# Performance work log

Measured on AMD Instinct MI355X. Metric: run time of the kernel, lower is better.

Reference implementation:

```python
import jax, jax.numpy as jnp
import numpy as np

INPUT_SIZE = 1024
HIDDEN_SIZE = 1024

def _xavier(key, shape):
    fan_in, fan_out = shape
    limit = np.sqrt(6.0 / (fan_in + fan_out))
    return jax.random.uniform(key, shape, jnp.float32, -limit, limit)

def setup_inputs() -> dict:
    key = jax.random.key(0)
    ks = jax.random.split(key, 9)
    x = jax.random.normal(ks[0], (64, 512, INPUT_SIZE), jnp.float32)
    d = {"x": x}
    names_i = ["W_ii", "W_fi", "W_gi", "W_oi"]
    names_h = ["W_ih", "W_fh", "W_gh", "W_oh"]
    for n, k in zip(names_i, ks[1:5]):
        d[n] = _xavier(k, (INPUT_SIZE, HIDDEN_SIZE))
    for n, k in zip(names_h, ks[5:9]):
        d[n] = _xavier(k, (HIDDEN_SIZE, HIDDEN_SIZE))
    for n in ["b_ii", "b_ih", "b_fi", "b_fh", "b_gi", "b_gh", "b_oi", "b_oh"]:
        d[n] = jnp.zeros((HIDDEN_SIZE,), jnp.float32)
    return d

def _lstm(x, W_ii, W_ih, b_ii, b_ih, W_fi, W_fh, b_fi, b_fh,
          W_gi, W_gh, b_gi, b_gh, W_oi, W_oh, b_oi, b_oh):
    B, S, _ = x.shape
    H = W_ih.shape[0]
    # Fuse the 4 input-side GEMMs into one and hoist out of the recurrence.
    Wi = jnp.concatenate([W_ii, W_fi, W_gi, W_oi], axis=1)          # [I, 4H]
    Wh = jnp.concatenate([W_ih, W_fh, W_gh, W_oh], axis=1)          # [H, 4H]
    bi = jnp.concatenate([b_ii + b_ih, b_fi + b_fh, b_gi + b_gh, b_oi + b_oh])
    xproj = jnp.einsum('bsi,ig->bsg', x, Wi) + bi                    # [B, S, 4H]

    def step(carry, xp_t):
        h, c = carry
        gates = xp_t + h @ Wh                                        # [B, 4H]
        i_t = jax.nn.sigmoid(gates[:, 0 * H:1 * H])
        f_t = jax.nn.sigmoid(gates[:, 1 * H:2 * H])
        g_t = jnp.tanh(gates[:, 2 * H:3 * H])
        o_t = jax.nn.sigmoid(gates[:, 3 * H:4 * H])
        c = f_t * c + i_t * g_t
        h = o_t * jnp.tanh(c)
        return (h, c), None

    h0 = jnp.zeros((B, H), x.dtype)
    c0 = jnp.zeros((B, H), x.dtype)
    (h_t, c_t), _ = jax.lax.scan(step, (h0, c0), jnp.swapaxes(xproj, 0, 1))
    return h_t, c_t

def reference(x, W_ii, W_ih, b_ii, b_ih, W_fi, W_fh, b_fi, b_fh,
              W_gi, W_gh, b_gi, b_gh, W_oi, W_oh, b_oi, b_oh):
    return _lstm(x, W_ii, W_ih, b_ii, b_ih, W_fi, W_fh, b_fi, b_fh,
                 W_gi, W_gh, b_gi, b_gh, W_oi, W_oh, b_oi, b_oh)
```

## Files before the change

kernel.cpp:

```cpp
#include <hip/hip_runtime.h>
#include <hip/hip_bf16.h>

#define SEQ   512
#define HID   1024
#define NBLK  256
#define NTHR  256
#define PADK  2056
#define GPS   36

typedef __attribute__((ext_vector_type(8))) short bf16x8;
typedef __attribute__((ext_vector_type(4))) float f32x4;
typedef __attribute__((ext_vector_type(2))) float f32x2;

struct Params {
  const float* x;
  const float* Wi[4];
  const float* Wh[4];
  const float* bi[4];
  const float* bh[4];
  float* out;
  const short* xbf;
  short* hb0;
  short* hb1;
  unsigned* arrive;
  unsigned* gen;
};

__device__ __forceinline__ float sig_(float v)  { return 1.0f / (1.0f + __expf(-v)); }
__device__ __forceinline__ float tanh_(float v) { return 1.0f - 2.0f / (__expf(2.0f * v) + 1.0f); }

__device__ __forceinline__ short f2b(float f) {
  unsigned u = __builtin_bit_cast(unsigned, f);
  u += 0x7FFFu + ((u >> 16) & 1u);
  return (short)(u >> 16);
}
__device__ __forceinline__ bf16x8 cvt8(const float* p) {
  f32x4 a = *(const f32x4*)p;
  f32x4 b = *(const f32x4*)(p + 4);
  bf16x8 r;
  r[0] = f2b(a[0]); r[1] = f2b(a[1]); r[2] = f2b(a[2]); r[3] = f2b(a[3]);
  r[4] = f2b(b[0]); r[5] = f2b(b[1]); r[6] = f2b(b[2]); r[7] = f2b(b[3]);
  return r;
}

__device__ __forceinline__ bf16x8 ld16_sc1(const short* p) {
  bf16x8 r;
  asm volatile("global_load_dwordx4 %0, %1, off sc1" : "=v"(r) : "v"(p));
  return r;
}
__device__ __forceinline__ void wait_vm0() {
  asm volatile("s_waitcnt vmcnt(0)" ::: "memory");
}

__global__ __launch_bounds__(256) void init_ws(unsigned* bar, unsigned* hzero, int hn) {
  int i = blockIdx.x * blockDim.x + threadIdx.x;
  if (i < 8448) bar[i] = 0u;
  if (i < hn) hzero[i] = 0u;
}

__global__ __launch_bounds__(256) void cvt_x(const float* __restrict__ x,
                                             short* __restrict__ xb) {
  size_t i = ((size_t)blockIdx.x * 256 + threadIdx.x) * 8;
  *(bf16x8*)(xb + i) = cvt8(x + i);
}

__device__ __forceinline__ void gbar_fence(unsigned* arrive, unsigned* gen,
                                           int tid, int bid, unsigned tgt) {
  __syncthreads();
  if (bid == 0) {
    if (tid != 0) {
      int polls = 0;
      while (__hip_atomic_load(&arrive[tid * 32], __ATOMIC_RELAXED,
                               __HIP_MEMORY_SCOPE_AGENT) < tgt) {
        __builtin_amdgcn_s_sleep(1);
        if (++polls > (1 << 22)) break;
      }
    }
    __syncthreads();
    if (tid == 0) {
      __threadfence();
      __hip_atomic_store(gen, tgt, __ATOMIC_RELEASE, __HIP_MEMORY_SCOPE_AGENT);
    }
    __syncthreads();
  } else {
    if (tid == 0) {
      __threadfence();
      __hip_atomic_store(&arrive[bid * 32], tgt, __ATOMIC_RELEASE,
                         __HIP_MEMORY_SCOPE_AGENT);
      int polls = 0;
      while (__hip_atomic_load(gen, __ATOMIC_RELAXED,
                               __HIP_MEMORY_SCOPE_AGENT) < tgt) {
        __builtin_amdgcn_s_sleep(1);
        if (++polls > (1 << 22)) break;
      }
      __threadfence();
    }
    __syncthreads();
  }
}

template <bool FULL>
__global__ __launch_bounds__(NTHR, 1) void lstm_persistent(Params p) {
  extern __shared__ char smem[];
  short* bls    = (short*)smem;
  float* gparts = (float*)(smem + 131584);
  float* cst    = (float*)(smem + 131584 + 18432);
  float* bias_s = (float*)(smem + 131584 + 18432 + 1024);

  const int tid = threadIdx.x;
  const int bid = blockIdx.x;
  const int cg  = bid & 127;
  const int mh  = bid >> 7;
  const int r0  = mh * 32;
  const int j0  = cg * 8;

  {
    const int g    = tid & 3;
    const int krow = tid >> 2;
    const float* wi = p.Wi[g];
    const float* wh = p.Wh[g];
    for (int kb = 0; kb < 2048; kb += 64) {
      int k = kb + krow;
      const float* src = (k < HID) ? (wi + (size_t)k * HID + j0)
                                   : (wh + (size_t)(k - HID) * HID + j0);
      f32x4 va = *(const f32x4*)src;
      f32x4 vb = *(const f32x4*)(src + 4);
      #pragma unroll
      for (int jj = 0; jj < 4; ++jj) {
        bls[(4 * jj + g) * PADK + k]       = f2b(va[jj]);
        bls[(4 * (jj + 4) + g) * PADK + k] = f2b(vb[jj]);
      }
    }
  }
  if (tid < 32) {
    int g = tid & 3, j = j0 + (tid >> 2);
    bias_s[tid] = p.bi[g][j] + p.bh[g][j];
  }
  if (tid < 128) { cst[2 * tid] = 0.0f; cst[2 * tid + 1] = 0.0f; }
  __syncthreads();

  const int lane = tid & 63;
  const int ksl  = tid >> 6;
  const int m16  = lane & 15;
  const int quad = lane >> 4;
  const size_t rm0 = (size_t)(r0 + m16);
  const size_t rm1 = (size_t)(r0 + 16 + m16);
  const short* bB0 = bls + (size_t)m16 * PADK + ksl * 512 + quad * 8;
  const short* bB1 = bls + (size_t)(16 + m16) * PADK + ksl * 512 + quad * 8;

  const unsigned* myflag =
      p.arrive + (size_t)(mh * 128 + (ksl - 2) * 64 + lane) * 32;

  float cfin0 = 0.0f, cfin1 = 0.0f;

  for (int t = 0; t < SEQ; ++t) {
    f32x4 acc00 = {0,0,0,0}, acc01 = {0,0,0,0};
    f32x4 acc10 = {0,0,0,0}, acc11 = {0,0,0,0};

    if constexpr (FULL) {
      if (ksl < 2) {
        const short* xb = p.xbf + ksl * 512 + quad * 8 + (size_t)t * HID;
        const short* pa0 = xb + rm0 * (SEQ * HID);
        const short* pa1 = xb + rm1 * (SEQ * HID);
        #pragma unroll 4
        for (int ki = 0; ki < 16; ++ki) {
          bf16x8 a0 = *(const bf16x8*)(pa0 + ki * 32);
          bf16x8 a1 = *(const bf16x8*)(pa1 + ki * 32);
          bf16x8 b0 = *(const bf16x8*)(bB0 + ki * 32);
          bf16x8 b1 = *(const bf16x8*)(bB1 + ki * 32);
          acc00 = __builtin_amdgcn_mfma_f32_16x16x32_bf16(a0, b0, acc00, 0, 0, 0);
          acc01 = __builtin_amdgcn_mfma_f32_16x16x32_bf16(a0, b1, acc01, 0, 0, 0);
          acc10 = __builtin_amdgcn_mfma_f32_16x16x32_bf16(a1, b0, acc10, 0, 0, 0);
          acc11 = __builtin_amdgcn_mfma_f32_16x16x32_bf16(a1, b1, acc11, 0, 0, 0);
        }
      } else {
        if (t > 0) {
          int polls = 0;
          while (__hip_atomic_load(myflag, __ATOMIC_RELAXED,
                                   __HIP_MEMORY_SCOPE_AGENT) < (unsigned)t) {
            __builtin_amdgcn_s_sleep(1);
            if (++polls > (1 << 22)) break;
          }
        }
        const short* hr = ((t & 1) ? p.hb1 : p.hb0) + (ksl - 2) * 512 + quad * 8;
        const short* pa0 = hr + rm0 * HID;
        const short* pa1 = hr + rm1 * HID;
        bf16x8 A0[16], A1[16];
        #pragma unroll
        for (int ki = 0; ki < 16; ++ki) {
          A0[ki] = ld16_sc1(pa0 + ki * 32);
          A1[ki] = ld16_sc1(pa1 + ki * 32);
        }
        wait_vm0();
        #pragma unroll
        for (int ki = 0; ki < 16; ++ki) {
          asm volatile("" : "+v"(A0[ki]));
          asm volatile("" : "+v"(A1[ki]));
        }
        #pragma unroll
        for (int ki = 0; ki < 16; ++ki) {
          bf16x8 b0 = *(const bf16x8*)(bB0 + ki * 32);
          bf16x8 b1 = *(const bf16x8*)(bB1 + ki * 32);
          acc00 = __builtin_amdgcn_mfma_f32_16x16x32_bf16(A0[ki], b0, acc00, 0, 0, 0);
          acc01 = __builtin_amdgcn_mfma_f32_16x16x32_bf16(A0[ki], b1, acc01, 0, 0, 0);
          acc10 = __builtin_amdgcn_mfma_f32_16x16x32_bf16(A1[ki], b0, acc10, 0, 0, 0);
          acc11 = __builtin_amdgcn_mfma_f32_16x16x32_bf16(A1[ki], b1, acc11, 0, 0, 0);
        }
      }
    } else {
      const float *fa0, *fa1;
      if (ksl < 2) {
        const float* xb = p.x + ksl * 512 + quad * 8 + (size_t)t * HID;
        fa0 = xb + rm0 * (SEQ * HID);
        fa1 = xb + rm1 * (SEQ * HID);
      } else {
        const float* hr = (p.out + ((t & 1) ? 65536 : 0)) + (ksl - 2) * 512 + quad * 8;
        fa0 = hr + rm0 * HID;
        fa1 = hr + rm1 * HID;
      }
      #pragma unroll 2
      for (int ki = 0; ki < 16; ++ki) {
        bf16x8 a0 = cvt8(fa0 + ki * 32);
        bf16x8 a1 = cvt8(fa1 + ki * 32);
        bf16x8 b0 = *(const bf16x8*)(bB0 + ki * 32);
        bf16x8 b1 = *(const bf16x8*)(bB1 + ki * 32);
        acc00 = __builtin_amdgcn_mfma_f32_16x16x32_bf16(a0, b0, acc00, 0, 0, 0);
        acc01 = __builtin_amdgcn_mfma_f32_16x16x32_bf16(a0, b1, acc01, 0, 0, 0);
        acc10 = __builtin_amdgcn_mfma_f32_16x16x32_bf16(a1, b0, acc10, 0, 0, 0);
        acc11 = __builtin_amdgcn_mfma_f32_16x16x32_bf16(a1, b1, acc11, 0, 0, 0);
      }
    }

    {
      float* gp = gparts + ksl * (32 * GPS);
      #pragma unroll
      for (int r = 0; r < 4; ++r) {
        gp[(quad * 4 + r) * GPS + m16]           = acc00[r];
        gp[(quad * 4 + r) * GPS + 16 + m16]      = acc01[r];
        gp[(16 + quad * 4 + r) * GPS + m16]      = acc10[r];
        gp[(16 + quad * 4 + r) * GPS + 16 + m16] = acc11[r];
      }
    }
    __syncthreads();

    if (tid < 128) {
      int rl = tid >> 2, jp = tid & 3;
      f32x4 ga = {0,0,0,0}, gb = {0,0,0,0};
      #pragma unroll
      for (int s = 0; s < 4; ++s) {
        const float* gp = gparts + s * (32 * GPS) + rl * GPS + jp * 8;
        ga += *(const f32x4*)gp;
        gb += *(const f32x4*)(gp + 4);
      }
      f32x4 ba = *(const f32x4*)(bias_s + jp * 8);
      f32x4 bb = *(const f32x4*)(bias_s + jp * 8 + 4);

      float i0 = sig_(ga[0] + ba[0]);
      float f0 = sig_(ga[1] + ba[1]);
      float g0 = tanh_(ga[2] + ba[2]);
      float o0 = sig_(ga[3] + ba[3]);
      float i1 = sig_(gb[0] + bb[0]);
      float f1 = sig_(gb[1] + bb[1]);
      float g1 = tanh_(gb[2] + bb[2]);
      float o1 = sig_(gb[3] + bb[3]);

      int ci = rl * 8 + jp * 2;
      float c0 = f0 * cst[ci]     + i0 * g0;
      float c1 = f1 * cst[ci + 1] + i1 * g1;
      cst[ci] = c0; cst[ci + 1] = c1;
      float h0v = o0 * tanh_(c0);
      float h1v = o1 * tanh_(c1);

      size_t off = (size_t)(r0 + rl) * HID + j0 + jp * 2;
      if constexpr (FULL) {
        short* hw = (t & 1) ? p.hb0 : p.hb1;
        unsigned u = (unsigned)(unsigned short)f2b(h0v) |
                     ((unsigned)(unsigned short)f2b(h1v) << 16);
        __hip_atomic_store((unsigned*)(hw + off), u, __ATOMIC_RELAXED,
                           __HIP_MEMORY_SCOPE_AGENT);
        if (t == SEQ - 1) {
          f32x2 hv = {h0v, h1v}; *(f32x2*)(p.out + off) = hv;
          f32x2 cv = {c0, c1};   *(f32x2*)(p.out + 65536 + off) = cv;
        }
      } else {
        float* hw = p.out + ((t & 1) ? 0 : 65536);
        f32x2 hv = {h0v, h1v};
        *(f32x2*)(hw + off) = hv;
        if (t == SEQ - 1) { cfin0 = c0; cfin1 = c1; }
      }
    }

    if constexpr (FULL) {
      __syncthreads();
      if (t < SEQ - 1 && tid == 0)
        __hip_atomic_store(&p.arrive[bid * 32], (unsigned)(t + 1),
                           __ATOMIC_RELAXED, __HIP_MEMORY_SCOPE_AGENT);
    } else {
      if (t < SEQ - 1)
        gbar_fence(p.arrive, p.gen, tid, bid, (unsigned)(t + 1));
    }
  }

  if constexpr (!FULL) {
    if (tid < 128) {
      int rl = tid >> 2, jp = tid & 3;
      size_t off = (size_t)(r0 + rl) * HID + j0 + jp * 2;
      f32x2 cv = {cfin0, cfin1};
      *(f32x2*)(p.out + 65536 + off) = cv;
    }
  }
}

extern "C" void kernel_launch(void* const* d_in, const int* in_sizes, int n_in,
                              void* d_out, int out_size, void* d_ws, size_t ws_size,
                              hipStream_t stream) {
  Params prm;
  prm.x = (const float*)d_in[0];
  for (int g = 0; g < 4; ++g) {
    prm.Wi[g] = (const float*)d_in[1 + g];
    prm.Wh[g] = (const float*)d_in[5 + g];
    prm.bi[g] = (const float*)d_in[9 + 2 * g];
    prm.bh[g] = (const float*)d_in[10 + 2 * g];
  }
  prm.out    = (float*)d_out;
  prm.arrive = (unsigned*)d_ws;
  prm.gen    = prm.arrive + 8192;
  prm.xbf = nullptr; prm.hb0 = nullptr; prm.hb1 = nullptr;

  const size_t need_full = 65536 + 67108864 + 2 * 131072;
  const bool full = ws_size >= need_full;
  if (full) {
    prm.xbf = (const short*)((char*)d_ws + 65536);
    prm.hb0 = (short*)((char*)d_ws + 65536 + 67108864);
    prm.hb1 = prm.hb0 + 65536;
  }

  const int smem_bytes = 131584 + 18432 + 1024 + 128;
  hipFuncSetAttribute((const void*)lstm_persistent<true>,
                      hipFuncAttributeMaxDynamicSharedMemorySize, smem_bytes);
  hipFuncSetAttribute((const void*)lstm_persistent<false>,
                      hipFuncAttributeMaxDynamicSharedMemorySize, smem_bytes);

  if (full) {
    init_ws<<<256, 256, 0, stream>>>((unsigned*)d_ws, (unsigned*)prm.hb0, 32768);
    cvt_x<<<16384, 256, 0, stream>>>(prm.x, (short*)prm.xbf);
    lstm_persistent<true><<<NBLK, NTHR, smem_bytes, stream>>>(prm);
  } else {
    init_ws<<<256, 256, 0, stream>>>((unsigned*)d_ws, (unsigned*)d_out, 65536);
    lstm_persistent<false><<<NBLK, NTHR, smem_bytes, stream>>>(prm);
  }
}
```

Baseline: 3.687 ms.

## Replace double-buffered h with per-step ring and drop x bf16 pre-conversion

Removes the separate cvt_x pass: x is read as fp32 and converted to bf16 inside the recurrence loop. It also replaces the ping-pong h buffers with a ring holding one slot per timestep. Because no slot is ever overwritten, h loads can drop the sc1 cache-bypass modifier and go through the normal cache path. The cost is twice as many bytes of x read per step, plus inline conversion work and a larger workspace requirement (512 slots).

```diff
diff --git a/kernel.cpp b/kernel.cpp
--- a/kernel.cpp
+++ b/kernel.cpp
@@ -7,6 +7,7 @@
 #define NTHR  256
 #define PADK  2056
 #define GPS   36
+#define RSLOT 65792
 
 typedef __attribute__((ext_vector_type(8))) short bf16x8;
 typedef __attribute__((ext_vector_type(4))) float f32x4;
@@ -19,9 +20,7 @@
   const float* bi[4];
   const float* bh[4];
   float* out;
-  const short* xbf;
-  short* hb0;
-  short* hb1;
+  short* hring;
   unsigned* arrive;
   unsigned* gen;
 };
@@ -43,9 +42,9 @@
   return r;
 }
 
-__device__ __forceinline__ bf16x8 ld16_sc1(const short* p) {
+__device__ __forceinline__ bf16x8 ld16_l2(const short* p) {
   bf16x8 r;
-  asm volatile("global_load_dwordx4 %0, %1, off sc1" : "=v"(r) : "v"(p));
+  asm volatile("global_load_dwordx4 %0, %1, off" : "=v"(r) : "v"(p));
   return r;
 }
 __device__ __forceinline__ void wait_vm0() {
@@ -56,12 +55,6 @@
   int i = blockIdx.x * blockDim.x + threadIdx.x;
   if (i < 8448) bar[i] = 0u;
   if (i < hn) hzero[i] = 0u;
-}
-
-__global__ __launch_bounds__(256) void cvt_x(const float* __restrict__ x,
-                                             short* __restrict__ xb) {
-  size_t i = ((size_t)blockIdx.x * 256 + threadIdx.x) * 8;
-  *(bf16x8*)(xb + i) = cvt8(x + i);
 }
 
 __device__ __forceinline__ void gbar_fence(unsigned* arrive, unsigned* gen,
@@ -159,13 +152,13 @@
 
     if constexpr (FULL) {
       if (ksl < 2) {
-        const short* xb = p.xbf + ksl * 512 + quad * 8 + (size_t)t * HID;
-        const short* pa0 = xb + rm0 * (SEQ * HID);
-        const short* pa1 = xb + rm1 * (SEQ * HID);
+        const float* xb = p.x + ksl * 512 + quad * 8 + (size_t)t * HID;
+        const float* fa0 = xb + rm0 * (SEQ * HID);
+        const float* fa1 = xb + rm1 * (SEQ * HID);
         #pragma unroll 4
         for (int ki = 0; ki < 16; ++ki) {
-          bf16x8 a0 = *(const bf16x8*)(pa0 + ki * 32);
-          bf16x8 a1 = *(const bf16x8*)(pa1 + ki * 32);
+          bf16x8 a0 = cvt8(fa0 + ki * 32);
+          bf16x8 a1 = cvt8(fa1 + ki * 32);
           bf16x8 b0 = *(const bf16x8*)(bB0 + ki * 32);
           bf16x8 b1 = *(const bf16x8*)(bB1 + ki * 32);
           acc00 = __builtin_amdgcn_mfma_f32_16x16x32_bf16(a0, b0, acc00, 0, 0, 0);
@@ -182,14 +175,15 @@
             if (++polls > (1 << 22)) break;
           }
         }
-        const short* hr = ((t & 1) ? p.hb1 : p.hb0) + (ksl - 2) * 512 + quad * 8;
+        const short* hr = p.hring + (size_t)t * RSLOT
+                        + (ksl - 2) * 512 + quad * 8;
         const short* pa0 = hr + rm0 * HID;
         const short* pa1 = hr + rm1 * HID;
         bf16x8 A0[16], A1[16];
         #pragma unroll
         for (int ki = 0; ki < 16; ++ki) {
-          A0[ki] = ld16_sc1(pa0 + ki * 32);
-          A1[ki] = ld16_sc1(pa1 + ki * 32);
+          A0[ki] = ld16_l2(pa0 + ki * 32);
+          A1[ki] = ld16_l2(pa1 + ki * 32);
         }
         wait_vm0();
         #pragma unroll
@@ -273,12 +267,13 @@
 
       size_t off = (size_t)(r0 + rl) * HID + j0 + jp * 2;
       if constexpr (FULL) {
-        short* hw = (t & 1) ? p.hb0 : p.hb1;
-        unsigned u = (unsigned)(unsigned short)f2b(h0v) |
-                     ((unsigned)(unsigned short)f2b(h1v) << 16);
-        __hip_atomic_store((unsigned*)(hw + off), u, __ATOMIC_RELAXED,
-                           __HIP_MEMORY_SCOPE_AGENT);
-        if (t == SEQ - 1) {
+        if (t < SEQ - 1) {
+          short* hw = p.hring + (size_t)(t + 1) * RSLOT;
+          unsigned u = (unsigned)(unsigned short)f2b(h0v) |
+                       ((unsigned)(unsigned short)f2b(h1v) << 16);
+          __hip_atomic_store((unsigned*)(hw + off), u, __ATOMIC_RELAXED,
+                             __HIP_MEMORY_SCOPE_AGENT);
+        } else {
           f32x2 hv = {h0v, h1v}; *(f32x2*)(p.out + off) = hv;
           f32x2 cv = {c0, c1};   *(f32x2*)(p.out + 65536 + off) = cv;
         }
@@ -325,15 +320,11 @@
   prm.out    = (float*)d_out;
   prm.arrive = (unsigned*)d_ws;
   prm.gen    = prm.arrive + 8192;
-  prm.xbf = nullptr; prm.hb0 = nullptr; prm.hb1 = nullptr;
-
-  const size_t need_full = 65536 + 67108864 + 2 * 131072;
+  prm.hring  = nullptr;
+
+  const size_t need_full = 65536 + (size_t)SEQ * (size_t)RSLOT * 2;
   const bool full = ws_size >= need_full;
-  if (full) {
-    prm.xbf = (const short*)((char*)d_ws + 65536);
-    prm.hb0 = (short*)((char*)d_ws + 65536 + 67108864);
-    prm.hb1 = prm.hb0 + 65536;
-  }
+  if (full) prm.hring = (short*)((char*)d_ws + 65536);
 
   const int smem_bytes = 131584 + 18432 + 1024 + 128;
   hipFuncSetAttribute((const void*)lstm_persistent<true>,
@@ -342,8 +333,7 @@
                       hipFuncAttributeMaxDynamicSharedMemorySize, smem_bytes);
 
   if (full) {
-    init_ws<<<256, 256, 0, stream>>>((unsigned*)d_ws, (unsigned*)prm.hb0, 32768);
-    cvt_x<<<16384, 256, 0, stream>>>(prm.x, (short*)prm.xbf);
+    init_ws<<<256, 256, 0, stream>>>((unsigned*)d_ws, (unsigned*)prm.hring, 32768);
     lstm_persistent<true><<<NBLK, NTHR, smem_bytes, stream>>>(prm);
   } else {
     init_ws<<<256, 256, 0, stream>>>((unsigned*)d_ws, (unsigned*)d_out, 65536);
```

Result: slower. 4.541 ms (+23.2%).

## Use per-timestep hidden-state ring buffer with plain loads and packed arrive flags

Applied to the files above, without the earlier changes.

Adds a mode that writes each step's bf16 hidden state into a separate ring slot, so readers can use ordinary cached global loads instead of sc1 loads. Fresh addresses each step avoid stale-cache hazards without bypass bits. It also packs the per-block arrive flags contiguously instead of spacing them 128 bytes apart. The cost is a larger workspace (512 slots), and the flag packing changes cache-line sharing among pollers and writers.

```diff
diff --git a/kernel.cpp b/kernel.cpp
--- a/kernel.cpp
+++ b/kernel.cpp
@@ -7,6 +7,7 @@
 #define NTHR  256
 #define PADK  2056
 #define GPS   36
+#define RSLOT 65792
 
 typedef __attribute__((ext_vector_type(8))) short bf16x8;
 typedef __attribute__((ext_vector_type(4))) float f32x4;
@@ -20,6 +21,7 @@
   const float* bh[4];
   float* out;
   const short* xbf;
+  short* hring;
   short* hb0;
   short* hb1;
   unsigned* arrive;
@@ -46,6 +48,11 @@
 __device__ __forceinline__ bf16x8 ld16_sc1(const short* p) {
   bf16x8 r;
   asm volatile("global_load_dwordx4 %0, %1, off sc1" : "=v"(r) : "v"(p));
+  return r;
+}
+__device__ __forceinline__ bf16x8 ld16_l2(const short* p) {
+  bf16x8 r;
+  asm volatile("global_load_dwordx4 %0, %1, off" : "=v"(r) : "v"(p));
   return r;
 }
 __device__ __forceinline__ void wait_vm0() {
@@ -99,7 +106,7 @@
   }
 }
 
-template <bool FULL>
+template <int MODE>
 __global__ __launch_bounds__(NTHR, 1) void lstm_persistent(Params p) {
   extern __shared__ char smem[];
   short* bls    = (short*)smem;
@@ -149,7 +156,7 @@
   const short* bB1 = bls + (size_t)(16 + m16) * PADK + ksl * 512 + quad * 8;
 
   const unsigned* myflag =
-      p.arrive + (size_t)(mh * 128 + (ksl - 2) * 64 + lane) * 32;
+      p.arrive + (size_t)(mh * 128 + (ksl - 2) * 64 + lane);
 
   float cfin0 = 0.0f, cfin1 = 0.0f;
 
@@ -157,7 +164,7 @@
     f32x4 acc00 = {0,0,0,0}, acc01 = {0,0,0,0};
     f32x4 acc10 = {0,0,0,0}, acc11 = {0,0,0,0};
 
-    if constexpr (FULL) {
+    if constexpr (MODE >= 1) {
       if (ksl < 2) {
         const short* xb = p.xbf + ksl * 512 + quad * 8 + (size_t)t * HID;
         const short* pa0 = xb + rm0 * (SEQ * HID);
@@ -182,14 +189,23 @@
             if (++polls > (1 << 22)) break;
           }
         }
-        const short* hr = ((t & 1) ? p.hb1 : p.hb0) + (ksl - 2) * 512 + quad * 8;
+        const short* hr;
+        if constexpr (MODE == 2)
+          hr = p.hring + (size_t)t * RSLOT + (ksl - 2) * 512 + quad * 8;
+        else
+          hr = ((t & 1) ? p.hb1 : p.hb0) + (ksl - 2) * 512 + quad * 8;
         const short* pa0 = hr + rm0 * HID;
         const short* pa1 = hr + rm1 * HID;
         bf16x8 A0[16], A1[16];
         #pragma unroll
         for (int ki = 0; ki < 16; ++ki) {
-          A0[ki] = ld16_sc1(pa0 + ki * 32);
-          A1[ki] = ld16_sc1(pa1 + ki * 32);
+          if constexpr (MODE == 2) {
+            A0[ki] = ld16_l2(pa0 + ki * 32);
+            A1[ki] = ld16_l2(pa1 + ki * 32);
+          } else {
+            A0[ki] = ld16_sc1(pa0 + ki * 32);
+            A1[ki] = ld16_sc1(pa1 + ki * 32);
+          }
         }
         wait_vm0();
         #pragma unroll
@@ -272,13 +288,18 @@
       float h1v = o1 * tanh_(c1);
 
       size_t off = (size_t)(r0 + rl) * HID + j0 + jp * 2;
-      if constexpr (FULL) {
-        short* hw = (t & 1) ? p.hb0 : p.hb1;
+      if constexpr (MODE >= 1) {
         unsigned u = (unsigned)(unsigned short)f2b(h0v) |
                      ((unsigned)(unsigned short)f2b(h1v) << 16);
-        __hip_atomic_store((unsigned*)(hw + off), u, __ATOMIC_RELAXED,
-                           __HIP_MEMORY_SCOPE_AGENT);
-        if (t == SEQ - 1) {
+        if (t < SEQ - 1) {
+          short* hw;
+          if constexpr (MODE == 2)
+            hw = p.hring + (size_t)(t + 1) * RSLOT;
+          else
+            hw = (t & 1) ? p.hb0 : p.hb1;
+          __hip_atomic_store((unsigned*)(hw + off), u, __ATOMIC_RELAXED,
+                             __HIP_MEMORY_SCOPE_AGENT);
+        } else {
           f32x2 hv = {h0v, h1v}; *(f32x2*)(p.out + off) = hv;
           f32x2 cv = {c0, c1};   *(f32x2*)(p.out + 65536 + off) = cv;
         }
@@ -290,10 +311,10 @@
       }
     }
 
-    if constexpr (FULL) {
+    if constexpr (MODE >= 1) {
       __syncthreads();
       if (t < SEQ - 1 && tid == 0)
-        __hip_atomic_store(&p.arrive[bid * 32], (unsigned)(t + 1),
+        __hip_atomic_store(&p.arrive[bid], (unsigned)(t + 1),
                            __ATOMIC_RELAXED, __HIP_MEMORY_SCOPE_AGENT);
     } else {
       if (t < SEQ - 1)
@@ -301,7 +322,7 @@
     }
   }
 
-  if constexpr (!FULL) {
+  if constexpr (MODE == 0) {
     if (tid < 128) {
       int rl = tid >> 2, jp = tid & 3;
       size_t off = (size_t)(r0 + rl) * HID + j0 + jp * 2;
@@ -325,28 +346,41 @@
   prm.out    = (float*)d_out;
   prm.arrive = (unsigned*)d_ws;
   prm.gen    = prm.arrive + 8192;
-  prm.xbf = nullptr; prm.hb0 = nullptr; prm.hb1 = nullptr;
-
-  const size_t need_full = 65536 + 67108864 + 2 * 131072;
-  const bool full = ws_size >= need_full;
-  if (full) {
-    prm.xbf = (const short*)((char*)d_ws + 65536);
-    prm.hb0 = (short*)((char*)d_ws + 65536 + 67108864);
+  prm.xbf = nullptr; prm.hring = nullptr; prm.hb0 = nullptr; prm.hb1 = nullptr;
+
+  const size_t XBF   = 67108864;
+  const size_t need_pp   = 65536 + XBF + 2 * 131072;
+  const size_t need_ring = 65536 + XBF + (size_t)SEQ * RSLOT * 2;
+  int mode = 0;
+  if (ws_size >= need_ring)      mode = 2;
+  else if (ws_size >= need_pp)   mode = 1;
+
+  if (mode >= 1) prm.xbf = (const short*)((char*)d_ws + 65536);
+  if (mode == 2) {
+    prm.hring = (short*)((char*)d_ws + 65536 + XBF);
+  } else if (mode == 1) {
+    prm.hb0 = (short*)((char*)d_ws + 65536 + XBF);
     prm.hb1 = prm.hb0 + 65536;
   }
 
   const int smem_bytes = 131584 + 18432 + 1024 + 128;
-  hipFuncSetAttribute((const void*)lstm_persistent<true>,
+  hipFuncSetAttribute((const void*)lstm_persistent<2>,
                       hipFuncAttributeMaxDynamicSharedMemorySize, smem_bytes);
-  hipFuncSetAttribute((const void*)lstm_persistent<false>,
+  hipFuncSetAttribute((const void*)lstm_persistent<1>,
                       hipFuncAttributeMaxDynamicSharedMemorySize, smem_bytes);
-
-  if (full) {
+  hipFuncSetAttribute((const void*)lstm_persistent<0>,
+                      hipFuncAttributeMaxDynamicSharedMemorySize, smem_bytes);
+
+  if (mode == 2) {
+    init_ws<<<256, 256, 0, stream>>>((unsigned*)d_ws, (unsigned*)prm.hring, 32768);
+    cvt_x<<<16384, 256, 0, stream>>>(prm.x, (short*)prm.xbf);
+    lstm_persistent<2><<<NBLK, NTHR, smem_bytes, stream>>>(prm);
+  } else if (mode == 1) {
     init_ws<<<256, 256, 0, stream>>>((unsigned*)d_ws, (unsigned*)prm.hb0, 32768);
     cvt_x<<<16384, 256, 0, stream>>>(prm.x, (short*)prm.xbf);
-    lstm_persistent<true><<<NBLK, NTHR, smem_bytes, stream>>>(prm);
+    lstm_persistent<1><<<NBLK, NTHR, smem_bytes, stream>>>(prm);
   } else {
     init_ws<<<256, 256, 0, stream>>>((unsigned*)d_ws, (unsigned*)d_out, 65536);
-    lstm_persistent<false><<<NBLK, NTHR, smem_bytes, stream>>>(prm);
-  }
-}
+    lstm_persistent<0><<<NBLK, NTHR, smem_bytes, stream>>>(prm);
+  }
+}
```

After: 4.149 ms. +12.5%, slower.

## Replace per-block arrival flags with shared per-half atomic counters for h dependencies

Applied to the files above, without the earlier changes.

Each consumer wave used to poll its own producer block's flag. Now every producer wave waits for its h stores to finish and then increments a shared counter covering its batch-half and column-half, and consumers poll one counter until it reaches 128 times t. This cuts the number of distinct flag lines polled and drops the separate per-block store after __syncthreads. In exchange it adds atomic contention on a few hot counters, and consumers may wait on a broader set of producers than they strictly depend on.

```diff
diff --git a/kernel.cpp b/kernel.cpp
--- a/kernel.cpp
+++ b/kernel.cpp
@@ -99,7 +99,7 @@
   }
 }
 
-template <bool FULL>
+template <int MODE>
 __global__ __launch_bounds__(NTHR, 1) void lstm_persistent(Params p) {
   extern __shared__ char smem[];
   short* bls    = (short*)smem;
@@ -148,8 +148,10 @@
   const short* bB0 = bls + (size_t)m16 * PADK + ksl * 512 + quad * 8;
   const short* bB1 = bls + (size_t)(16 + m16) * PADK + ksl * 512 + quad * 8;
 
-  const unsigned* myflag =
-      p.arrive + (size_t)(mh * 128 + (ksl - 2) * 64 + lane) * 32;
+  unsigned* mycnt =
+      p.arrive + (size_t)(mh * 2 + ((ksl - 2) & 1)) * 32;
+  unsigned* prodcnt =
+      p.arrive + (size_t)(mh * 2 + (cg >> 6)) * 32;
 
   float cfin0 = 0.0f, cfin1 = 0.0f;
 
@@ -157,7 +159,7 @@
     f32x4 acc00 = {0,0,0,0}, acc01 = {0,0,0,0};
     f32x4 acc10 = {0,0,0,0}, acc11 = {0,0,0,0};
 
-    if constexpr (FULL) {
+    if constexpr (MODE == 1) {
       if (ksl < 2) {
         const short* xb = p.xbf + ksl * 512 + quad * 8 + (size_t)t * HID;
         const short* pa0 = xb + rm0 * (SEQ * HID);
@@ -173,11 +175,12 @@
           acc10 = __builtin_amdgcn_mfma_f32_16x16x32_bf16(a1, b0, acc10, 0, 0, 0);
           acc11 = __builtin_amdgcn_mfma_f32_16x16x32_bf16(a1, b1, acc11, 0, 0, 0);
         }
-      } else {
-        if (t > 0) {
+      } else if (t > 0) {
+        {
+          const unsigned tgt = 128u * (unsigned)t;
           int polls = 0;
-          while (__hip_atomic_load(myflag, __ATOMIC_RELAXED,
-                                   __HIP_MEMORY_SCOPE_AGENT) < (unsigned)t) {
+          while (__hip_atomic_load(mycnt, __ATOMIC_RELAXED,
+                                   __HIP_MEMORY_SCOPE_AGENT) < tgt) {
             __builtin_amdgcn_s_sleep(1);
             if (++polls > (1 << 22)) break;
           }
@@ -272,13 +275,18 @@
       float h1v = o1 * tanh_(c1);
 
       size_t off = (size_t)(r0 + rl) * HID + j0 + jp * 2;
-      if constexpr (FULL) {
-        short* hw = (t & 1) ? p.hb0 : p.hb1;
-        unsigned u = (unsigned)(unsigned short)f2b(h0v) |
-                     ((unsigned)(unsigned short)f2b(h1v) << 16);
-        __hip_atomic_store((unsigned*)(hw + off), u, __ATOMIC_RELAXED,
-                           __HIP_MEMORY_SCOPE_AGENT);
-        if (t == SEQ - 1) {
+      if constexpr (MODE == 1) {
+        if (t < SEQ - 1) {
+          short* hw = (t & 1) ? p.hb0 : p.hb1;
+          unsigned u = (unsigned)(unsigned short)f2b(h0v) |
+                       ((unsigned)(unsigned short)f2b(h1v) << 16);
+          __hip_atomic_store((unsigned*)(hw + off), u, __ATOMIC_RELAXED,
+                             __HIP_MEMORY_SCOPE_AGENT);
+          wait_vm0();
+          if ((tid & 63) == 0)
+            (void)__hip_atomic_fetch_add(prodcnt, 1u, __ATOMIC_RELAXED,
+                                         __HIP_MEMORY_SCOPE_AGENT);
+        } else {
           f32x2 hv = {h0v, h1v}; *(f32x2*)(p.out + off) = hv;
           f32x2 cv = {c0, c1};   *(f32x2*)(p.out + 65536 + off) = cv;
         }
@@ -290,18 +298,15 @@
       }
     }
 
-    if constexpr (FULL) {
+    if constexpr (MODE == 1) {
       __syncthreads();
-      if (t < SEQ - 1 && tid == 0)
-        __hip_atomic_store(&p.arrive[bid * 32], (unsigned)(t + 1),
-                           __ATOMIC_RELAXED, __HIP_MEMORY_SCOPE_AGENT);
     } else {
       if (t < SEQ - 1)
         gbar_fence(p.arrive, p.gen, tid, bid, (unsigned)(t + 1));
     }
   }
 
-  if constexpr (!FULL) {
+  if constexpr (MODE == 0) {
     if (tid < 128) {
       int rl = tid >> 2, jp = tid & 3;
       size_t off = (size_t)(r0 + rl) * HID + j0 + jp * 2;
@@ -327,26 +332,28 @@
   prm.gen    = prm.arrive + 8192;
   prm.xbf = nullptr; prm.hb0 = nullptr; prm.hb1 = nullptr;
 
-  const size_t need_full = 65536 + 67108864 + 2 * 131072;
-  const bool full = ws_size >= need_full;
-  if (full) {
+  const size_t XBF   = 67108864;
+  const size_t need1 = 65536 + XBF + 2 * 131072;
+  const int mode = (ws_size >= need1) ? 1 : 0;
+
+  if (mode == 1) {
     prm.xbf = (const short*)((char*)d_ws + 65536);
-    prm.hb0 = (short*)((char*)d_ws + 65536 + 67108864);
+    prm.hb0 = (short*)((char*)d_ws + 65536 + XBF);
     prm.hb1 = prm.hb0 + 65536;
   }
 
   const int smem_bytes = 131584 + 18432 + 1024 + 128;
-  hipFuncSetAttribute((const void*)lstm_persistent<true>,
+  hipFuncSetAttribute((const void*)lstm_persistent<1>,
                       hipFuncAttributeMaxDynamicSharedMemorySize, smem_bytes);
-  hipFuncSetAttribute((const void*)lstm_persistent<false>,
+  hipFuncSetAttribute((const void*)lstm_persistent<0>,
                       hipFuncAttributeMaxDynamicSharedMemorySize, smem_bytes);
 
-  if (full) {
+  if (mode == 1) {
     init_ws<<<256, 256, 0, stream>>>((unsigned*)d_ws, (unsigned*)prm.hb0, 32768);
     cvt_x<<<16384, 256, 0, stream>>>(prm.x, (short*)prm.xbf);
-    lstm_persistent<true><<<NBLK, NTHR, smem_bytes, stream>>>(prm);
+    lstm_persistent<1><<<NBLK, NTHR, smem_bytes, stream>>>(prm);
   } else {
     init_ws<<<256, 256, 0, stream>>>((unsigned*)d_ws, (unsigned*)d_out, 65536);
-    lstm_persistent<false><<<NBLK, NTHR, smem_bytes, stream>>>(prm);
-  }
-}
+    lstm_persistent<0><<<NBLK, NTHR, smem_bytes, stream>>>(prm);
+  }
+}
```

Result: slower. 5.315 ms (+44.2%).
